# Optimization experiments

Hardware: AMD Instinct MI355X
Metric: run time of the kernel (lower is better)

Reference implementation:

```python
import jax, jax.numpy as jnp
import numpy as np

N = 50000
IN_DIM = 256
HID = 64
HEADS = 4
OUT_DIM = 64
NEG_SLOPE = 0.2


def gat_conv(x, src, dst, W, att_src, att_dst, bias, heads, out_ch):
    # x: [N, F_in]; src/dst: [E] (self-loops already appended)
    n = x.shape[0]
    h = (x @ W).reshape(n, heads, out_ch)                     # [N,H,C]
    a_s = jnp.sum(h * att_src, axis=-1)                       # [N,H]
    a_d = jnp.sum(h * att_dst, axis=-1)                       # [N,H]
    e = jax.nn.leaky_relu(a_s[src] + a_d[dst], NEG_SLOPE)     # [E,H]
    # segment softmax over destination neighborhoods
    m = jax.ops.segment_max(e, dst, num_segments=n)           # [N,H]
    m = jnp.where(jnp.isfinite(m), m, 0.0)
    ex = jnp.exp(e - m[dst])                                  # [E,H]
    denom = jax.ops.segment_sum(ex, dst, num_segments=n)      # [N,H]
    alpha = ex / (denom[dst] + 1e-16)                         # [E,H]
    msg = alpha[:, :, None] * h[src]                          # [E,H,C]
    out = jax.ops.segment_sum(msg, dst, num_segments=n)       # [N,H,C]
    return out.reshape(n, heads * out_ch) + bias


def setup_inputs() -> dict:
    key = jax.random.key(0)
    ks = jax.random.split(key, 10)
    glorot = lambda k, shape: jax.random.normal(k, shape, jnp.float32) * np.sqrt(2.0 / (shape[0] + shape[-1]))
    x = jax.random.normal(ks[0], (N, IN_DIM), jnp.float32)
    edge_index = jax.random.randint(ks[1], (2, 800000), 0, N, jnp.int64)
    W1 = glorot(ks[2], (IN_DIM, HEADS * HID))
    att_src1 = glorot(ks[3], (HEADS, HID))
    att_dst1 = glorot(ks[4], (HEADS, HID))
    b1 = jnp.zeros((HEADS * HID,), jnp.float32)
    W2 = glorot(ks[5], (HEADS * HID, OUT_DIM))
    att_src2 = glorot(ks[6], (1, OUT_DIM))
    att_dst2 = glorot(ks[7], (1, OUT_DIM))
    b2 = jnp.zeros((OUT_DIM,), jnp.float32)
    return {"x": x, "edge_index": edge_index, "W1": W1, "att_src1": att_src1,
            "att_dst1": att_dst1, "b1": b1, "W2": W2, "att_src2": att_src2,
            "att_dst2": att_dst2, "b2": b2}


def reference(x, edge_index, W1, att_src1, att_dst1, b1, W2, att_src2, att_dst2, b2):
    # add self loops (PyG GATConv default)
    loops = jnp.arange(N, dtype=edge_index.dtype)
    src = jnp.concatenate([edge_index[0], loops])
    dst = jnp.concatenate([edge_index[1], loops])
    h = gat_conv(x, src, dst, W1, att_src1, att_dst1, b1, HEADS, HID)
    h = jax.nn.elu(h)
    out = gat_conv(h, src, dst, W2, att_src2, att_dst2, b2, 1, OUT_DIM)
    return out
```

## Files before the change

### kernel.cpp

```cpp
#include <hip/hip_runtime.h>
#include <math.h>

#define N_NODES 50000
#define E_RAW   800000
#define E_TOT   850000
#define NEG_SLOPE 0.2f
#define NBC 196

typedef __attribute__((ext_vector_type(8))) short short8;
typedef __attribute__((ext_vector_type(4))) float f32x4;

__device__ __forceinline__ float lrelu(float v) {
    return v >= 0.f ? v : NEG_SLOPE * v;
}
__device__ __forceinline__ unsigned short f2bf(float f) {
    union { float f; unsigned u; } v; v.f = f;
    unsigned r = v.u + 0x7FFF + ((v.u >> 16) & 1);
    return (unsigned short)(r >> 16);
}
__device__ __forceinline__ float bf2f(unsigned short h) {
    union { unsigned u; float f; } v; v.u = ((unsigned)h) << 16;
    return v.f;
}
__device__ __forceinline__ int C1(int p) { return (p & 15) * 16 + (p >> 4); }
__device__ __forceinline__ int C2(int p) { return (p & 3) * 16 + (p >> 2); }

__global__ __launch_bounds__(256) void k_prep_hist(
    const int* __restrict__ dst, int* __restrict__ counts,
    const float* __restrict__ W1, const float* __restrict__ W2,
    unsigned short* __restrict__ Wf1, unsigned short* __restrict__ Wf2)
{
    int idx = blockIdx.x * 256 + threadIdx.x;
    if (idx < 8192) {
        int lane = idx & 63, kb = (idx >> 6) & 7, nb = idx >> 9;
        int c = nb * 16 + (lane & 15);
        int k0 = kb * 32 + ((lane >> 4) & 3) * 8;
        short8 pk;
#pragma unroll
        for (int j = 0; j < 8; ++j)
            pk[j] = (short)f2bf(W1[(k0 + j) * 256 + c]);
        *(short8*)&Wf1[idx * 8] = pk;
    } else if (idx < 10240) {
        int i2 = idx - 8192;
        int lane = i2 & 63, kb = (i2 >> 6) & 7, nb = i2 >> 9;
        int c = nb * 16 + (lane & 15);
        int k0 = kb * 32 + ((lane >> 4) & 3) * 8;
        short8 pk;
#pragma unroll
        for (int j = 0; j < 8; ++j)
            pk[j] = (short)f2bf(W2[C1(k0 + j) * 64 + c]);
        *(short8*)&Wf2[i2 * 8] = pk;
    }
    if (idx < E_TOT) {
        int d = (idx < E_RAW) ? dst[idx] : idx - E_RAW;
        atomicAdd(&counts[d], 1);
    }
}

__global__ __launch_bounds__(256) void k_scan1(
    const int* __restrict__ counts, int* __restrict__ off, int* __restrict__ bsum)
{
    __shared__ int sh[256];
    int t = threadIdx.x, i = blockIdx.x * 256 + t;
    int c = (i < N_NODES) ? counts[i] : 0;
    sh[t] = c; __syncthreads();
    for (int ofs = 1; ofs < 256; ofs <<= 1) {
        int v = (t >= ofs) ? sh[t - ofs] : 0;
        __syncthreads(); sh[t] += v; __syncthreads();
    }
    if (i < N_NODES) off[i] = sh[t] - c;
    if (t == 255) bsum[blockIdx.x] = sh[255];
}

__global__ __launch_bounds__(256) void k_scan2(int* __restrict__ bsum)
{
    __shared__ int sh[256];
    int t = threadIdx.x;
    int c = (t < NBC) ? bsum[t] : 0;
    sh[t] = c; __syncthreads();
    for (int ofs = 1; ofs < 256; ofs <<= 1) {
        int v = (t >= ofs) ? sh[t - ofs] : 0;
        __syncthreads(); sh[t] += v; __syncthreads();
    }
    if (t < NBC) bsum[t] = sh[t] - c;
}

__global__ __launch_bounds__(256) void k_scan3(
    int* __restrict__ off, const int* __restrict__ bsum)
{
    int i = blockIdx.x * 256 + threadIdx.x;
    if (i < N_NODES) off[i] += bsum[blockIdx.x];
    if (i == 0) off[N_NODES] = E_TOT;
}

__global__ __launch_bounds__(256) void k_scatter(
    const int* __restrict__ src, const int* __restrict__ dst,
    const int* __restrict__ off, int* __restrict__ cursor,
    unsigned short* __restrict__ esrc)
{
    int e = blockIdx.x * 256 + threadIdx.x;
    if (e >= E_TOT) return;
    int s, d;
    if (e < E_RAW) { s = src[e]; d = dst[e]; } else { s = e - E_RAW; d = s; }
    int pos = off[d] + atomicAdd(&cursor[d], 1);
    esrc[pos] = (unsigned short)s;
}

__global__ __launch_bounds__(256) void k_gemm1(
    const float* __restrict__ x, const unsigned short* __restrict__ Wf1,
    const float* __restrict__ att_src, const float* __restrict__ att_dst,
    unsigned short* __restrict__ h1b, float* __restrict__ as1, float* __restrict__ ad1)
{
    const int t = threadIdx.x;
    const int lane = t & 63;
    const int w = t >> 6;
    const int rbase = blockIdx.x * 16;
    const int q  = lane & 15;
    const int kg = lane >> 4;
    const int rowA = rbase + q;

    f32x4 acc[4];
#pragma unroll
    for (int nb = 0; nb < 4; ++nb) acc[nb] = (f32x4){0.f, 0.f, 0.f, 0.f};

    short8 b[2][4];
    float4 a0, a1, a0n, a1n;
    {
        const float* ap = &x[rowA * 256 + kg * 8];
        a0 = *(const float4*)ap;
        a1 = *(const float4*)(ap + 4);
#pragma unroll
        for (int nb = 0; nb < 4; ++nb)
            b[0][nb] = *(const short8*)&Wf1[(((w * 4 + nb) * 8 + 0) * 64 + lane) * 8];
    }
#pragma unroll
    for (int kb = 0; kb < 8; ++kb) {
        if (kb < 7) {
            const float* ap = &x[rowA * 256 + (kb + 1) * 32 + kg * 8];
            a0n = *(const float4*)ap;
            a1n = *(const float4*)(ap + 4);
#pragma unroll
            for (int nb = 0; nb < 4; ++nb)
                b[(kb + 1) & 1][nb] =
                    *(const short8*)&Wf1[(((w * 4 + nb) * 8 + kb + 1) * 64 + lane) * 8];
        }
        short8 af;
        af[0] = (short)f2bf(a0.x); af[1] = (short)f2bf(a0.y);
        af[2] = (short)f2bf(a0.z); af[3] = (short)f2bf(a0.w);
        af[4] = (short)f2bf(a1.x); af[5] = (short)f2bf(a1.y);
        af[6] = (short)f2bf(a1.z); af[7] = (short)f2bf(a1.w);
#pragma unroll
        for (int nb = 0; nb < 4; ++nb)
            acc[nb] = __builtin_amdgcn_mfma_f32_16x16x32_bf16(af, b[kb & 1][nb], acc[nb], 0, 0, 0);
        if (kb < 7) { a0 = a0n; a1 = a1n; }
    }

#pragma unroll
    for (int reg = 0; reg < 4; ++reg) {
        int n = rbase + kg * 4 + reg;
        ushort4 pk;
        pk.x = f2bf(acc[0][reg]); pk.y = f2bf(acc[1][reg]);
        pk.z = f2bf(acc[2][reg]); pk.w = f2bf(acc[3][reg]);
        *(ushort4*)&h1b[n * 256 + q * 16 + w * 4] = pk;
    }
    float asv[4], adv[4];
#pragma unroll
    for (int nb = 0; nb < 4; ++nb) {
        int col = (w * 4 + nb) * 16 + q;
        asv[nb] = att_src[col];
        adv[nb] = att_dst[col];
    }
#pragma unroll
    for (int reg = 0; reg < 4; ++reg) {
        float s = acc[0][reg]*asv[0] + acc[1][reg]*asv[1] + acc[2][reg]*asv[2] + acc[3][reg]*asv[3];
        float d = acc[0][reg]*adv[0] + acc[1][reg]*adv[1] + acc[2][reg]*adv[2] + acc[3][reg]*adv[3];
#pragma unroll
        for (int ofs = 1; ofs < 16; ofs <<= 1) {
            s += __shfl_xor(s, ofs);
            d += __shfl_xor(d, ofs);
        }
        if (q == 0) {
            int n = rbase + kg * 4 + reg;
            as1[n * 4 + w] = s;
            ad1[n * 4 + w] = d;
        }
    }
}

__global__ __launch_bounds__(256) void k_gat1g2(
    const unsigned short* __restrict__ esrc, const int* __restrict__ off,
    const float* __restrict__ as1, const float* __restrict__ ad1,
    const unsigned short* __restrict__ h1b, const float* __restrict__ b1,
    const unsigned short* __restrict__ Wf2,
    const float* __restrict__ att_src2, const float* __restrict__ att_dst2,
    unsigned short* __restrict__ h2b, float* __restrict__ as2, float* __restrict__ ad2)
{
    __shared__ unsigned short hs[16][264];
    __shared__ float ss[16][4], sd[16][4];
    const int t = threadIdx.x;
    const int w = t >> 6;
    const int lane = t & 63;
    const int d0 = blockIdx.x * 16;
    const int head = lane & 3;

    for (int r = 0; r < 4; ++r) {
        const int ld = w * 4 + r;
        const int d = d0 + ld;
        const float adv = ad1[d * 4 + head];
        const int e0 = off[d], e1 = off[d + 1];
        float4 acc = make_float4(0.f, 0.f, 0.f, 0.f);
        float dn = 0.f;
        int e = e0;
        for (; e + 3 < e1; e += 4) {
            int s0 = esrc[e], s1 = esrc[e + 1], s2 = esrc[e + 2], s3 = esrc[e + 3];
            float w0 = __expf(lrelu(as1[s0 * 4 + head] + adv));
            float w1 = __expf(lrelu(as1[s1 * 4 + head] + adv));
            float w2 = __expf(lrelu(as1[s2 * 4 + head] + adv));
            float w3 = __expf(lrelu(as1[s3 * 4 + head] + adv));
            ushort4 u0 = *(const ushort4*)&h1b[s0 * 256 + lane * 4];
            ushort4 u1 = *(const ushort4*)&h1b[s1 * 256 + lane * 4];
            ushort4 u2 = *(const ushort4*)&h1b[s2 * 256 + lane * 4];
            ushort4 u3 = *(const ushort4*)&h1b[s3 * 256 + lane * 4];
            dn += (w0 + w1) + (w2 + w3);
            acc.x = fmaf(w0, bf2f(u0.x), fmaf(w1, bf2f(u1.x), fmaf(w2, bf2f(u2.x), fmaf(w3, bf2f(u3.x), acc.x))));
            acc.y = fmaf(w0, bf2f(u0.y), fmaf(w1, bf2f(u1.y), fmaf(w2, bf2f(u2.y), fmaf(w3, bf2f(u3.y), acc.y))));
            acc.z = fmaf(w0, bf2f(u0.z), fmaf(w1, bf2f(u1.z), fmaf(w2, bf2f(u2.z), fmaf(w3, bf2f(u3.z), acc.z))));
            acc.w = fmaf(w0, bf2f(u0.w), fmaf(w1, bf2f(u1.w), fmaf(w2, bf2f(u2.w), fmaf(w3, bf2f(u3.w), acc.w))));
        }
        for (; e < e1; ++e) {
            int s0 = esrc[e];
            float w0 = __expf(lrelu(as1[s0 * 4 + head] + adv));
            ushort4 u0 = *(const ushort4*)&h1b[s0 * 256 + lane * 4];
            dn += w0;
            acc.x = fmaf(w0, bf2f(u0.x), acc.x);
            acc.y = fmaf(w0, bf2f(u0.y), acc.y);
            acc.z = fmaf(w0, bf2f(u0.z), acc.z);
            acc.w = fmaf(w0, bf2f(u0.w), acc.w);
        }
        const float inv = 1.f / (dn + 1e-16f);
        float o[4] = {acc.x, acc.y, acc.z, acc.w};
        ushort4 pk;
        unsigned short* pko = (unsigned short*)&pk;
#pragma unroll
        for (int i = 0; i < 4; ++i) {
            float v = o[i] * inv + b1[C1(lane * 4 + i)];
            v = v > 0.f ? v : expm1f(v);
            pko[i] = f2bf(v);
        }
        *(ushort4*)&hs[ld][lane * 4] = pk;
    }
    __syncthreads();

    const int q  = lane & 15;
    const int kg = lane >> 4;
    f32x4 acc2 = (f32x4){0.f, 0.f, 0.f, 0.f};
#pragma unroll
    for (int kb = 0; kb < 8; ++kb) {
        short8 af = *(const short8*)&hs[q][kb * 32 + kg * 8];
        short8 bf = *(const short8*)&Wf2[((w * 8 + kb) * 64 + lane) * 8];
        acc2 = __builtin_amdgcn_mfma_f32_16x16x32_bf16(af, bf, acc2, 0, 0, 0);
    }
    const float asv = att_src2[w * 16 + q];
    const float adv = att_dst2[w * 16 + q];
#pragma unroll
    for (int reg = 0; reg < 4; ++reg) {
        int row = kg * 4 + reg;
        int n = d0 + row;
        h2b[n * 64 + q * 4 + w] = f2bf(acc2[reg]);
        float s = acc2[reg] * asv;
        float d = acc2[reg] * adv;
#pragma unroll
        for (int ofs = 1; ofs < 16; ofs <<= 1) {
            s += __shfl_xor(s, ofs);
            d += __shfl_xor(d, ofs);
        }
        if (q == 0) { ss[row][w] = s; sd[row][w] = d; }
    }
    __syncthreads();
    if (t < 16) {
        as2[d0 + t] = (ss[t][0] + ss[t][1]) + (ss[t][2] + ss[t][3]);
        ad2[d0 + t] = (sd[t][0] + sd[t][1]) + (sd[t][2] + sd[t][3]);
    }
}

__global__ __launch_bounds__(256) void k_gather2(
    const unsigned short* __restrict__ esrc, const int* __restrict__ off,
    const float* __restrict__ as2, const float* __restrict__ ad2,
    const unsigned short* __restrict__ h2b, const float* __restrict__ b2,
    float* __restrict__ out)
{
    const int t = threadIdx.x;
    const int w = t >> 6;
    const int lane = t & 63;
    const int g  = lane >> 4;
    const int j2 = lane & 15;
    const int d = blockIdx.x * 16 + w * 4 + g;
    const float adv = ad2[d];
    const int e0 = off[d], e1 = off[d + 1];
    const unsigned short* hb = h2b + j2 * 4;

    float acc[4] = {0.f, 0.f, 0.f, 0.f};
    float dn = 0.f;
    int e = e0;
    for (; e + 3 < e1; e += 4) {
        int s0 = esrc[e], s1 = esrc[e + 1], s2 = esrc[e + 2], s3 = esrc[e + 3];
        float w0 = __expf(lrelu(as2[s0] + adv));
        float w1 = __expf(lrelu(as2[s1] + adv));
        float w2 = __expf(lrelu(as2[s2] + adv));
        float w3 = __expf(lrelu(as2[s3] + adv));
        ushort4 u0 = *(const ushort4*)(hb + s0 * 64);
        ushort4 u1 = *(const ushort4*)(hb + s1 * 64);
        ushort4 u2 = *(const ushort4*)(hb + s2 * 64);
        ushort4 u3 = *(const ushort4*)(hb + s3 * 64);
        dn += (w0 + w1) + (w2 + w3);
        acc[0] = fmaf(w0, bf2f(u0.x), fmaf(w1, bf2f(u1.x), fmaf(w2, bf2f(u2.x), fmaf(w3, bf2f(u3.x), acc[0]))));
        acc[1] = fmaf(w0, bf2f(u0.y), fmaf(w1, bf2f(u1.y), fmaf(w2, bf2f(u2.y), fmaf(w3, bf2f(u3.y), acc[1]))));
        acc[2] = fmaf(w0, bf2f(u0.z), fmaf(w1, bf2f(u1.z), fmaf(w2, bf2f(u2.z), fmaf(w3, bf2f(u3.z), acc[2]))));
        acc[3] = fmaf(w0, bf2f(u0.w), fmaf(w1, bf2f(u1.w), fmaf(w2, bf2f(u2.w), fmaf(w3, bf2f(u3.w), acc[3]))));
    }
    for (; e < e1; ++e) {
        int s0 = esrc[e];
        float w0 = __expf(lrelu(as2[s0] + adv));
        ushort4 u0 = *(const ushort4*)(hb + s0 * 64);
        dn += w0;
        acc[0] = fmaf(w0, bf2f(u0.x), acc[0]);
        acc[1] = fmaf(w0, bf2f(u0.y), acc[1]);
        acc[2] = fmaf(w0, bf2f(u0.z), acc[2]);
        acc[3] = fmaf(w0, bf2f(u0.w), acc[3]);
    }
    const float inv = 1.f / (dn + 1e-16f);
#pragma unroll
    for (int i = 0; i < 4; ++i) {
        int col = i * 16 + j2;
        out[d * 64 + col] = acc[i] * inv + b2[col];
    }
}

extern "C" void kernel_launch(void* const* d_in, const int* in_sizes, int n_in,
                              void* d_out, int out_size, void* d_ws, size_t ws_size,
                              hipStream_t stream)
{
    const float* x        = (const float*)d_in[0];
    const int*   ei       = (const int*)d_in[1];
    const float* W1       = (const float*)d_in[2];
    const float* att_src1 = (const float*)d_in[3];
    const float* att_dst1 = (const float*)d_in[4];
    const float* b1       = (const float*)d_in[5];
    const float* W2       = (const float*)d_in[6];
    const float* att_src2 = (const float*)d_in[7];
    const float* att_dst2 = (const float*)d_in[8];
    const float* b2       = (const float*)d_in[9];
    const int* src = ei;
    const int* dst = ei + E_RAW;
    float* out = (float*)d_out;

    char* ws = (char*)d_ws;
    int*            counts = (int*)(ws + 0);
    int*            cursor = (int*)(ws + 200000);
    int*            off    = (int*)(ws + 400032);
    int*            bsum   = (int*)(ws + 600064);
    float*          as1    = (float*)(ws + 600896);
    float*          ad1    = (float*)(ws + 1400896);
    float*          as2    = (float*)(ws + 2200896);
    float*          ad2    = (float*)(ws + 2400896);
    unsigned short* esrc   = (unsigned short*)(ws + 2600896);
    unsigned short* Wf1    = (unsigned short*)(ws + 4300896);
    unsigned short* Wf2    = (unsigned short*)(ws + 4431968);
    unsigned short* h1b    = (unsigned short*)(ws + 4464736);
    unsigned short* h2b    = (unsigned short*)(ws + 30064736);

    hipMemsetAsync(ws, 0, 400000, stream);

    const int EB = (E_TOT + 255) / 256;
    k_prep_hist<<<EB, 256, 0, stream>>>(dst, counts, W1, W2, Wf1, Wf2);
    k_scan1  <<<NBC, 256, 0, stream>>>(counts, off, bsum);
    k_scan2  <<<1, 256, 0, stream>>>(bsum);
    k_scan3  <<<NBC, 256, 0, stream>>>(off, bsum);
    k_scatter<<<EB, 256, 0, stream>>>(src, dst, off, cursor, esrc);
    k_gemm1  <<<3125, 256, 0, stream>>>(x, Wf1, att_src1, att_dst1, h1b, as1, ad1);
    k_gat1g2 <<<3125, 256, 0, stream>>>(esrc, off, as1, ad1, h1b, b1, Wf2,
                                        att_src2, att_dst2, h2b, as2, ad2);
    k_gather2<<<3125, 256, 0, stream>>>(esrc, off, as2, ad2, h2b, b2, out);
}
```

Before: 242.6 us.

## Fuse scan stages and co-schedule edge scatter with first GEMM

Merges the second and third scan kernels into one, where each block reduces the preceding block sums itself. The edge scatter is folded into the GEMM1 launch as extra blocks. It now decrements the histogram counts instead of using a separate zeroed cursor array, which also halves the memset. The goal is fewer kernel launches and letting the latency-bound scatter atomics overlap the compute-bound GEMM, at the cost of redundant per-block reductions and a different order within each CSR segment.

```diff
diff --git a/kernel.cpp b/kernel.cpp
--- a/kernel.cpp
+++ b/kernel.cpp
@@ -6,6 +6,8 @@
 #define E_TOT   850000
 #define NEG_SLOPE 0.2f
 #define NBC 196
+#define GEMM1_BLKS 3125
+#define SCAT_BLKS  3321
 
 typedef __attribute__((ext_vector_type(8))) short short8;
 typedef __attribute__((ext_vector_type(4))) float f32x4;
@@ -72,45 +74,41 @@
     if (t == 255) bsum[blockIdx.x] = sh[255];
 }
 
-__global__ __launch_bounds__(256) void k_scan2(int* __restrict__ bsum)
+__global__ __launch_bounds__(256) void k_scan23(
+    int* __restrict__ off, const int* __restrict__ bsum)
 {
     __shared__ int sh[256];
-    int t = threadIdx.x;
-    int c = (t < NBC) ? bsum[t] : 0;
-    sh[t] = c; __syncthreads();
-    for (int ofs = 1; ofs < 256; ofs <<= 1) {
-        int v = (t >= ofs) ? sh[t - ofs] : 0;
-        __syncthreads(); sh[t] += v; __syncthreads();
-    }
-    if (t < NBC) bsum[t] = sh[t] - c;
-}
-
-__global__ __launch_bounds__(256) void k_scan3(
-    int* __restrict__ off, const int* __restrict__ bsum)
-{
-    int i = blockIdx.x * 256 + threadIdx.x;
-    if (i < N_NODES) off[i] += bsum[blockIdx.x];
-    if (i == 0) off[N_NODES] = E_TOT;
-}
-
-__global__ __launch_bounds__(256) void k_scatter(
-    const int* __restrict__ src, const int* __restrict__ dst,
-    const int* __restrict__ off, int* __restrict__ cursor,
-    unsigned short* __restrict__ esrc)
-{
-    int e = blockIdx.x * 256 + threadIdx.x;
-    if (e >= E_TOT) return;
-    int s, d;
-    if (e < E_RAW) { s = src[e]; d = dst[e]; } else { s = e - E_RAW; d = s; }
-    int pos = off[d] + atomicAdd(&cursor[d], 1);
-    esrc[pos] = (unsigned short)s;
-}
-
-__global__ __launch_bounds__(256) void k_gemm1(
+    int t = threadIdx.x, b = blockIdx.x;
+    sh[t] = (t < b) ? bsum[t] : 0;
+    __syncthreads();
+    for (int ofs = 128; ofs > 0; ofs >>= 1) {
+        if (t < ofs) sh[t] += sh[t + ofs];
+        __syncthreads();
+    }
+    int base = sh[0];
+    int i = b * 256 + t;
+    if (i < N_NODES) off[i] += base;
+    if (b == 0 && t == 0) off[N_NODES] = E_TOT;
+}
+
+__global__ __launch_bounds__(256) void k_gemm1_scatter(
     const float* __restrict__ x, const unsigned short* __restrict__ Wf1,
     const float* __restrict__ att_src, const float* __restrict__ att_dst,
-    unsigned short* __restrict__ h1b, float* __restrict__ as1, float* __restrict__ ad1)
-{
+    unsigned short* __restrict__ h1b, float* __restrict__ as1, float* __restrict__ ad1,
+    const int* __restrict__ src, const int* __restrict__ dst,
+    const int* __restrict__ off, int* __restrict__ counts,
+    unsigned short* __restrict__ esrc)
+{
+    if (blockIdx.x >= GEMM1_BLKS) {
+        int e = (blockIdx.x - GEMM1_BLKS) * 256 + threadIdx.x;
+        if (e < E_TOT) {
+            int s, d;
+            if (e < E_RAW) { s = src[e]; d = dst[e]; } else { s = e - E_RAW; d = s; }
+            int old = atomicSub(&counts[d], 1);
+            esrc[off[d] + old - 1] = (unsigned short)s;
+        }
+        return;
+    }
     const int t = threadIdx.x;
     const int lane = t & 63;
     const int w = t >> 6;
@@ -356,28 +354,27 @@
 
     char* ws = (char*)d_ws;
     int*            counts = (int*)(ws + 0);
-    int*            cursor = (int*)(ws + 200000);
-    int*            off    = (int*)(ws + 400032);
-    int*            bsum   = (int*)(ws + 600064);
-    float*          as1    = (float*)(ws + 600896);
-    float*          ad1    = (float*)(ws + 1400896);
-    float*          as2    = (float*)(ws + 2200896);
-    float*          ad2    = (float*)(ws + 2400896);
-    unsigned short* esrc   = (unsigned short*)(ws + 2600896);
-    unsigned short* Wf1    = (unsigned short*)(ws + 4300896);
-    unsigned short* Wf2    = (unsigned short*)(ws + 4431968);
-    unsigned short* h1b    = (unsigned short*)(ws + 4464736);
-    unsigned short* h2b    = (unsigned short*)(ws + 30064736);
-
-    hipMemsetAsync(ws, 0, 400000, stream);
+    int*            off    = (int*)(ws + 200000);
+    int*            bsum   = (int*)(ws + 400032);
+    float*          as1    = (float*)(ws + 400896);
+    float*          ad1    = (float*)(ws + 1200896);
+    float*          as2    = (float*)(ws + 2000896);
+    float*          ad2    = (float*)(ws + 2200896);
+    unsigned short* esrc   = (unsigned short*)(ws + 2400896);
+    unsigned short* Wf1    = (unsigned short*)(ws + 4100896);
+    unsigned short* Wf2    = (unsigned short*)(ws + 4231968);
+    unsigned short* h1b    = (unsigned short*)(ws + 4264736);
+    unsigned short* h2b    = (unsigned short*)(ws + 29864736);
+
+    hipMemsetAsync(counts, 0, 200000, stream);
 
     const int EB = (E_TOT + 255) / 256;
     k_prep_hist<<<EB, 256, 0, stream>>>(dst, counts, W1, W2, Wf1, Wf2);
     k_scan1  <<<NBC, 256, 0, stream>>>(counts, off, bsum);
-    k_scan2  <<<1, 256, 0, stream>>>(bsum);
-    k_scan3  <<<NBC, 256, 0, stream>>>(off, bsum);
-    k_scatter<<<EB, 256, 0, stream>>>(src, dst, off, cursor, esrc);
-    k_gemm1  <<<3125, 256, 0, stream>>>(x, Wf1, att_src1, att_dst1, h1b, as1, ad1);
+    k_scan23 <<<NBC, 256, 0, stream>>>(off, bsum);
+    k_gemm1_scatter<<<GEMM1_BLKS + SCAT_BLKS, 256, 0, stream>>>(
+        x, Wf1, att_src1, att_dst1, h1b, as1, ad1,
+        src, dst, off, counts, esrc);
     k_gat1g2 <<<3125, 256, 0, stream>>>(esrc, off, as1, ad1, h1b, b1, Wf2,
                                         att_src2, att_dst2, h2b, as2, ad2);
     k_gather2<<<3125, 256, 0, stream>>>(esrc, off, as2, ad2, h2b, b2, out);
```

Result: faster. 234.2 us (-3.4%).
